# Performance work log

Measured on AMD Instinct MI355X. Metric: run time of the kernel, lower is better.

The kernel has to match this reference:

```python
import jax, jax.numpy as jnp
import numpy as np

B, S, D, H, WIN = 2, 2048, 1024, 16, 128
DH = D // H


def setup_inputs() -> dict:
    key = jax.random.key(0)
    ks = jax.random.split(key, 6)
    sc = D ** -0.5
    return {
        "x": jax.random.normal(ks[0], (B, S, D), jnp.float32),
        "in_proj_w": jax.random.normal(ks[1], (3 * D, D), jnp.float32) * sc,
        "in_proj_b": jnp.zeros((3 * D,), jnp.float32),
        "out_proj_w": jax.random.normal(ks[2], (D, D), jnp.float32) * sc,
        "out_proj_b": jnp.zeros((D,), jnp.float32),
        "ln1_g": jnp.ones((D,), jnp.float32),
        "ln1_b": jnp.zeros((D,), jnp.float32),
        "spec_wr": jax.random.normal(ks[3], (S // 2 + 1, D), jnp.float32) * 0.02 + 1.0,
        "spec_wi": jax.random.normal(ks[4], (S // 2 + 1, D), jnp.float32) * 0.02,
        "ln2_g": jnp.ones((D,), jnp.float32),
        "ln2_b": jnp.zeros((D,), jnp.float32),
    }


def _layernorm(x, g, b, eps=1e-5):
    mu = jnp.mean(x, axis=-1, keepdims=True)
    var = jnp.mean(jnp.square(x - mu), axis=-1, keepdims=True)
    return (x - mu) * jax.lax.rsqrt(var + eps) * g + b


def reference(x, in_proj_w, in_proj_b, out_proj_w, out_proj_b,
              ln1_g, ln1_b, spec_wr, spec_wi, ln2_g, ln2_b):
    b, s, d = x.shape
    # --- sliding-window MHA (torch nn.MultiheadAttention math) ---
    qkv = x @ in_proj_w.T + in_proj_b            # [B,S,3D]
    q, k, v = jnp.split(qkv, 3, axis=-1)
    q = q.reshape(b, s, H, DH)
    k = k.reshape(b, s, H, DH)
    v = v.reshape(b, s, H, DH)
    scores = jnp.einsum('bqhd,bkhd->bhqk', q, k) * (DH ** -0.5)
    idx = jnp.arange(s)
    band_mask = jnp.abs(idx[:, None] - idx[None, :]) > WIN  # True = masked
    scores = jnp.where(band_mask[None, None], -jnp.inf, scores)
    probs = jax.nn.softmax(scores, axis=-1)
    attn = jnp.einsum('bhqk,bkhd->bqhd', probs, v).reshape(b, s, d)
    attn_out = attn @ out_proj_w.T + out_proj_b
    x_attn = _layernorm(x + attn_out, ln1_g, ln1_b)
    # --- spectral block: rfft along seq, learned complex filter, irfft ---
    Xf = jnp.fft.rfft(x, axis=1)                  # [B, S//2+1, D] complex
    Wc = spec_wr + 1j * spec_wi
    x_wave = jnp.fft.irfft(Xf * Wc[None], n=s, axis=1).astype(x.dtype)
    # --- mix ---
    return _layernorm(x_attn + x_wave, ln2_g, ln2_b)
```

## Files before the change

kernel.cpp:

```cpp
#include <hip/hip_runtime.h>
#include <hip/hip_bf16.h>
#include <math.h>

#define BB    2
#define SS    2048
#define DD    1024
#define HH    16
#define DHH   64
#define WINW  128
#define MROWS (BB * SS)

typedef __attribute__((ext_vector_type(8))) short short8;
typedef __attribute__((ext_vector_type(4))) short short4v;
typedef __attribute__((ext_vector_type(4))) float floatx4;

__global__ __launch_bounds__(256) void transpose_x_cast(
    const float* __restrict__ src, float* __restrict__ dstT,
    __hip_bfloat16* __restrict__ dst_bf) {
  __shared__ float tile[64][65];
  const size_t base = (size_t)blockIdx.z * SS * DD;
  const int c0 = blockIdx.x * 64;
  const int r0 = blockIdx.y * 64;
  const int tx = threadIdx.x & 63;
  const int ty = threadIdx.x >> 6;
#pragma unroll
  for (int i = 0; i < 16; ++i) {
    const int r = ty * 16 + i;
    const float v = src[base + (size_t)(r0 + r) * DD + c0 + tx];
    tile[r][tx] = v;
    dst_bf[base + (size_t)(r0 + r) * DD + c0 + tx] = __float2bfloat16(v);
  }
  __syncthreads();
#pragma unroll
  for (int i = 0; i < 16; ++i) {
    const int c = ty * 16 + i;
    dstT[base + (size_t)(c0 + c) * SS + r0 + tx] = tile[tx][c];
  }
}

__global__ __launch_bounds__(256) void cast_w(
    const float* __restrict__ w_in, const float* __restrict__ w_out,
    __hip_bfloat16* __restrict__ o_in, __hip_bfloat16* __restrict__ o_out) {
  const int i = (blockIdx.x * 256 + threadIdx.x) * 4;
  const float* src; __hip_bfloat16* dst; int j;
  if (i < 3 * DD * DD) { src = w_in; dst = o_in; j = i; }
  else { src = w_out; dst = o_out; j = i - 3 * DD * DD; }
  const float4 v = *(const float4*)(src + j);
  dst[j + 0] = __float2bfloat16(v.x);
  dst[j + 1] = __float2bfloat16(v.y);
  dst[j + 2] = __float2bfloat16(v.z);
  dst[j + 3] = __float2bfloat16(v.w);
}

__global__ __launch_bounds__(256) void transpose_wrwi(
    const float* __restrict__ wr, const float* __restrict__ wi,
    float* __restrict__ wrT, float* __restrict__ wiT) {
  __shared__ float tile[64][65];
  const float* src = blockIdx.z ? wi : wr;
  float* dst = blockIdx.z ? wiT : wrT;
  const int R = 1025, C = DD;
  const int c0 = blockIdx.x * 64;
  const int r0 = blockIdx.y * 64;
  const int tx = threadIdx.x & 63;
  const int ty = threadIdx.x >> 6;
#pragma unroll
  for (int i = 0; i < 16; ++i) {
    const int r = ty * 16 + i;
    if (r0 + r < R) tile[r][tx] = src[(size_t)(r0 + r) * C + c0 + tx];
  }
  __syncthreads();
#pragma unroll
  for (int i = 0; i < 16; ++i) {
    const int c = ty * 16 + i;
    if (r0 + tx < R) dst[(size_t)(c0 + c) * R + r0 + tx] = tile[tx][c];
  }
}

__global__ __launch_bounds__(256) void transpose_f32(
    const float* __restrict__ src, float* __restrict__ dst, int R, int C) {
  __shared__ float tile[64][65];
  const size_t base = (size_t)blockIdx.z * R * C;
  const int c0 = blockIdx.x * 64;
  const int r0 = blockIdx.y * 64;
  const int tx = threadIdx.x & 63;
  const int ty = threadIdx.x >> 6;
#pragma unroll
  for (int i = 0; i < 16; ++i) {
    const int r = ty * 16 + i;
    tile[r][tx] = src[base + (size_t)(r0 + r) * C + c0 + tx];
  }
  __syncthreads();
#pragma unroll
  for (int i = 0; i < 16; ++i) {
    const int c = ty * 16 + i;
    dst[base + (size_t)(c0 + c) * R + r0 + tx] = tile[tx][c];
  }
}

__device__ inline void load16_lds(const __hip_bfloat16* g, __hip_bfloat16* l) {
  __builtin_amdgcn_global_load_lds(
      (const __attribute__((address_space(1))) uint32_t*)g,
      (__attribute__((address_space(3))) uint32_t*)l, 16, 0, 0);
}

#define GEMM_BODY(STORE)                                                       \
  __shared__ __attribute__((aligned(16))) __hip_bfloat16 As[128 * 32];         \
  __shared__ __attribute__((aligned(16))) __hip_bfloat16 Bs[128 * 32];         \
  const int tid  = threadIdx.x;                                                \
  const int lane = tid & 63;                                                   \
  const int wave = tid >> 6;                                                   \
  const int wrow = (wave >> 1) * 64;                                           \
  const int wcol = (wave & 1) * 64;                                            \
  int id_ = blockIdx.y * gridDim.x + blockIdx.x;                               \
  const int per_ = (gridDim.x * gridDim.y) >> 3;                               \
  id_ = (id_ & 7) * per_ + (id_ >> 3);                                         \
  const int row0 = (id_ & 31) * 128;                                           \
  const int col0 = (id_ >> 5) * 128;                                           \
  const int srow = tid >> 2;                                                   \
  const int skk  = (tid & 3) * 8;                                              \
  const int quad = lane >> 4;                                                  \
  const int l16  = lane & 15;                                                  \
  floatx4 acc[4][4] = {};                                                      \
  for (int k0 = 0; k0 < K; k0 += 32) {                                         \
    __syncthreads();                                                           \
    load16_lds(A + (size_t)(row0 + srow) * K + k0 + skk,      &As[tid * 8]);   \
    load16_lds(A + (size_t)(row0 + 64 + srow) * K + k0 + skk, &As[2048 + tid * 8]); \
    load16_lds(B + (size_t)(col0 + srow) * K + k0 + skk,      &Bs[tid * 8]);   \
    load16_lds(B + (size_t)(col0 + 64 + srow) * K + k0 + skk, &Bs[2048 + tid * 8]); \
    __syncthreads();                                                           \
    short8 af[4], bf[4];                                                       \
    _Pragma("unroll")                                                          \
    for (int i = 0; i < 4; ++i)                                                \
      af[i] = *(const short8*)&As[(wrow + i * 16 + l16) * 32 + quad * 8];      \
    _Pragma("unroll")                                                          \
    for (int j = 0; j < 4; ++j)                                                \
      bf[j] = *(const short8*)&Bs[(wcol + j * 16 + l16) * 32 + quad * 8];      \
    _Pragma("unroll")                                                          \
    for (int i = 0; i < 4; ++i)                                                \
      _Pragma("unroll")                                                        \
      for (int j = 0; j < 4; ++j)                                              \
        acc[i][j] = __builtin_amdgcn_mfma_f32_16x16x32_bf16(af[i], bf[j], acc[i][j], 0, 0, 0); \
  }                                                                            \
  _Pragma("unroll")                                                            \
  for (int i = 0; i < 4; ++i) {                                                \
    _Pragma("unroll")                                                          \
    for (int j = 0; j < 4; ++j) {                                              \
      const int col = col0 + wcol + j * 16 + l16;                              \
      const float bs = bias[col];                                              \
      _Pragma("unroll")                                                        \
      for (int r = 0; r < 4; ++r) {                                            \
        const int row = row0 + wrow + i * 16 + quad * 4 + r;                   \
        STORE;                                                                 \
      }                                                                        \
    }                                                                          \
  }

__global__ __launch_bounds__(256) void gemm_bf16_nt(
    const __hip_bfloat16* __restrict__ A, const __hip_bfloat16* __restrict__ B,
    const float* __restrict__ bias, float* __restrict__ C,
    int M, int N, int K) {
  GEMM_BODY(C[(size_t)row * N + col] = acc[i][j][r] + bs)
}

__global__ __launch_bounds__(256) void gemm_bf16_nt_bf16out(
    const __hip_bfloat16* __restrict__ A, const __hip_bfloat16* __restrict__ B,
    const float* __restrict__ bias, __hip_bfloat16* __restrict__ C,
    int M, int N, int K) {
  GEMM_BODY(C[(size_t)row * N + col] = __float2bfloat16(acc[i][j][r] + bs))
}

__global__ __launch_bounds__(256, 2) void attn_mfma(
    const __hip_bfloat16* __restrict__ qkv, __hip_bfloat16* __restrict__ attn) {
  __shared__ __attribute__((aligned(16))) __hip_bfloat16 QsA[64 * 32];
  __shared__ __attribute__((aligned(16))) __hip_bfloat16 QsB[64 * 32];
  __shared__ __attribute__((aligned(16))) __hip_bfloat16 KsA[160 * 32];
  __shared__ __attribute__((aligned(16))) __hip_bfloat16 KsB[160 * 32];
  __shared__ __attribute__((aligned(16))) __hip_bfloat16 Vt[64 * 168];
  __shared__ __attribute__((aligned(16))) __hip_bfloat16 Ps[64 * 168];

  const int tid  = threadIdx.x;
  const int lane = tid & 63;
  const int w    = tid >> 6;
  const int quad = lane >> 4;
  const int l16  = lane & 15;
  const int q0   = blockIdx.x * 64;
  const int h    = blockIdx.y;
  const int b    = blockIdx.z;
  const int kbase = q0 - WINW;

  const int r_ = tid >> 2;
  const int c8 = (tid & 3) * 8;

  {
    const __hip_bfloat16* src = qkv + ((size_t)(b * SS + q0 + r_)) * (3 * DD) + h * DHH;
    load16_lds(src + c8,      &QsA[r_ * 32 + c8]);
    load16_lds(src + 32 + c8, &QsB[r_ * 32 + c8]);
  }

  short8 qf0, qf1;
  float m_run[4] = {-1e30f, -1e30f, -1e30f, -1e30f};
  float l_run[4] = {0.f, 0.f, 0.f, 0.f};
  floatx4 ob[4] = {};

  for (int c = 0; c < 2; ++c) {
    const int ck0 = kbase + c * 160;
    __syncthreads();
#pragma unroll
    for (int it = 0; it < 3; ++it) {
      const int r = it * 64 + r_;
      if (r < 160) {
        int key = ck0 + r; key = key < 0 ? 0 : (key > SS - 1 ? SS - 1 : key);
        const __hip_bfloat16* src = qkv + ((size_t)(b * SS + key)) * (3 * DD) + DD + h * DHH;
        load16_lds(src + c8,      &KsA[r * 32 + c8]);
        load16_lds(src + 32 + c8, &KsB[r * 32 + c8]);
      }
    }
    {
      const int k4 = (tid >> 3) * 4;
      const int d8 = (tid & 7) * 8;
#pragma unroll
      for (int it = 0; it < 2; ++it) {
        const int rr = it * 128 + k4;
        if (rr < 160) {
          short8 v[4];
#pragma unroll
          for (int u = 0; u < 4; ++u) {
            int key = ck0 + rr + u; key = key < 0 ? 0 : (key > SS - 1 ? SS - 1 : key);
            v[u] = *(const short8*)(qkv + ((size_t)(b * SS + key)) * (3 * DD) + 2 * DD + h * DHH + d8);
          }
#pragma unroll
          for (int j = 0; j < 8; ++j) {
            short4v pk; pk[0] = v[0][j]; pk[1] = v[1][j]; pk[2] = v[2][j]; pk[3] = v[3][j];
            *(short4v*)&Vt[(d8 + j) * 168 + rr] = pk;
          }
        }
      }
    }
    __syncthreads();

    if (c == 0) {
      qf0 = *(const short8*)&QsA[(w * 16 + l16) * 32 + quad * 8];
      qf1 = *(const short8*)&QsB[(w * 16 + l16) * 32 + quad * 8];
    }

    floatx4 sc[10];
#pragma unroll
    for (int kt = 0; kt < 10; ++kt) {
      const short8 bk0 = *(const short8*)&KsA[(kt * 16 + l16) * 32 + quad * 8];
      const short8 bk1 = *(const short8*)&KsB[(kt * 16 + l16) * 32 + quad * 8];
      floatx4 a = {};
      a = __builtin_amdgcn_mfma_f32_16x16x32_bf16(qf0, bk0, a, 0, 0, 0);
      a = __builtin_amdgcn_mfma_f32_16x16x32_bf16(qf1, bk1, a, 0, 0, 0);
      sc[kt] = a;
    }

    float cm[4] = {-1e30f, -1e30f, -1e30f, -1e30f};
#pragma unroll
    for (int kt = 0; kt < 10; ++kt) {
      const int key = ck0 + kt * 16 + l16;
#pragma unroll
      for (int r = 0; r < 4; ++r) {
        const int qq = q0 + w * 16 + quad * 4 + r;
        const int dqk = qq - key;
        const bool ok = (key >= 0) & (key < SS) & (dqk <= WINW) & (dqk >= -WINW);
        const float s = ok ? sc[kt][r] * 0.125f : -1e30f;
        sc[kt][r] = s;
        cm[r] = fmaxf(cm[r], s);
      }
    }
#pragma unroll
    for (int off = 1; off < 16; off <<= 1)
#pragma unroll
      for (int r = 0; r < 4; ++r) cm[r] = fmaxf(cm[r], __shfl_xor(cm[r], off, 64));

    float alpha[4], csum[4] = {0.f, 0.f, 0.f, 0.f};
#pragma unroll
    for (int r = 0; r < 4; ++r) {
      const float mn = fmaxf(m_run[r], cm[r]);
      alpha[r] = __expf(m_run[r] - mn);
      m_run[r] = mn;
    }

    __hip_bfloat16* Pw = &Ps[w * 16 * 168];
#pragma unroll
    for (int kt = 0; kt < 10; ++kt) {
#pragma unroll
      for (int r = 0; r < 4; ++r) {
        const float p = __expf(sc[kt][r] - m_run[r]);
        csum[r] += p;
        Pw[(quad * 4 + r) * 168 + kt * 16 + l16] = __float2bfloat16(p);
      }
    }
#pragma unroll
    for (int off = 1; off < 16; off <<= 1)
#pragma unroll
      for (int r = 0; r < 4; ++r) csum[r] += __shfl_xor(csum[r], off, 64);
#pragma unroll
    for (int r = 0; r < 4; ++r) l_run[r] = l_run[r] * alpha[r] + csum[r];
#pragma unroll
    for (int t = 0; t < 4; ++t)
#pragma unroll
      for (int r = 0; r < 4; ++r) ob[t][r] *= alpha[r];

#pragma unroll
    for (int kt = 0; kt < 5; ++kt) {
      const short8 pf = *(const short8*)&Pw[l16 * 168 + kt * 32 + quad * 8];
#pragma unroll
      for (int t = 0; t < 4; ++t) {
        const short8 vf = *(const short8*)&Vt[(t * 16 + l16) * 168 + kt * 32 + quad * 8];
        ob[t] = __builtin_amdgcn_mfma_f32_16x16x32_bf16(pf, vf, ob[t], 0, 0, 0);
      }
    }
  }

  float inv[4];
#pragma unroll
  for (int r = 0; r < 4; ++r) inv[r] = 1.f / l_run[r];
  const int qq0 = q0 + w * 16 + quad * 4;
#pragma unroll
  for (int t = 0; t < 4; ++t)
#pragma unroll
    for (int r = 0; r < 4; ++r)
      attn[((size_t)(b * SS + qq0 + r)) * DD + h * DHH + t * 16 + l16] =
          __float2bfloat16(ob[t][r] * inv[r]);
}

__global__ __launch_bounds__(256) void add_ln(
    const float* __restrict__ a, const float* __restrict__ b,
    const float* __restrict__ g, const float* __restrict__ be,
    float* __restrict__ out) {
  const int row = blockIdx.x;
  const int tid = threadIdx.x;
  const int lane = tid & 63;
  const int wave = tid >> 6;

  const float4 av = *(const float4*)(a + (size_t)row * DD + tid * 4);
  const float4 bv = *(const float4*)(b + (size_t)row * DD + tid * 4);
  float v[4] = {av.x + bv.x, av.y + bv.y, av.z + bv.z, av.w + bv.w};

  float s = v[0] + v[1] + v[2] + v[3];
  float s2 = v[0] * v[0] + v[1] * v[1] + v[2] * v[2] + v[3] * v[3];
#pragma unroll
  for (int off = 32; off; off >>= 1) {
    s += __shfl_xor(s, off, 64);
    s2 += __shfl_xor(s2, off, 64);
  }
  __shared__ float red[8];
  if (lane == 0) { red[wave] = s; red[4 + wave] = s2; }
  __syncthreads();
  s = red[0] + red[1] + red[2] + red[3];
  s2 = red[4] + red[5] + red[6] + red[7];

  const float mu = s * (1.f / DD);
  const float var = s2 * (1.f / DD) - mu * mu;
  const float r = rsqrtf(var + 1e-5f);

  const float4 gv = *(const float4*)(g + tid * 4);
  const float4 bev = *(const float4*)(be + tid * 4);
  float4 o;
  o.x = (v[0] - mu) * r * gv.x + bev.x;
  o.y = (v[1] - mu) * r * gv.y + bev.y;
  o.z = (v[2] - mu) * r * gv.z + bev.z;
  o.w = (v[3] - mu) * r * gv.w + bev.w;
  *(float4*)(out + (size_t)row * DD + tid * 4) = o;
}

#define PADI(a) ((a) + ((a) >> 5))

__global__ __launch_bounds__(256) void spec_fft_pair(
    float* __restrict__ xT, const float* __restrict__ wrT,
    const float* __restrict__ wiT) {
  __shared__ float re[SS + SS / 32], im[SS + SS / 32];
  const int tid = threadIdx.x;
  const int d0 = blockIdx.x * 2, d1 = d0 + 1;
  const int b = blockIdx.y;
  float* col0 = xT + ((size_t)b * DD + d0) * SS;
  float* col1 = xT + ((size_t)b * DD + d1) * SS;

  for (int s4 = tid * 4; s4 < SS; s4 += 1024) {
    const float4 a = *(const float4*)(col0 + s4);
    const float4 c = *(const float4*)(col1 + s4);
    const int p = PADI(s4);
    re[p] = a.x; re[p + 1] = a.y; re[p + 2] = a.z; re[p + 3] = a.w;
    im[p] = c.x; im[p + 1] = c.y; im[p + 2] = c.z; im[p + 3] = c.w;
  }

  for (int stage = 11; stage >= 1; --stage) {
    __syncthreads();
    const int half = 1 << (stage - 1);
    const float ang0 = -6.283185307179586f / (float)(1 << stage);
#pragma unroll 4
    for (int t = tid; t < SS / 2; t += 256) {
      const int gI = t >> (stage - 1);
      const int p = t & (half - 1);
      const int i = (gI << stage) + p;
      const int j = i + half;
      float sn, cs;
      __sincosf(ang0 * (float)p, &sn, &cs);
      const int ii = PADI(i), jj = PADI(j);
      const float ar = re[ii], ai = im[ii], br = re[jj], bi = im[jj];
      re[ii] = ar + br; im[ii] = ai + bi;
      const float dr = ar - br, di = ai - bi;
      re[jj] = dr * cs - di * sn;
      im[jj] = dr * sn + di * cs;
    }
  }
  __syncthreads();

  const float* w0r = wrT + (size_t)d0 * 1025;
  const float* w0i = wiT + (size_t)d0 * 1025;
  const float* w1r = wrT + (size_t)d1 * 1025;
  const float* w1i = wiT + (size_t)d1 * 1025;
  const float sc = 1.0f / (float)SS;
  for (int k = tid; k < 1024; k += 256) {
    if (k == 0) {
      re[0] *= w0r[0] * sc;
      im[0] *= w1r[0] * sc;
      re[1] *= w0r[1024] * sc;
      im[1] *= w1r[1024] * sc;
    } else {
      const int p1 = PADI(__brev((unsigned)k) >> 21);
      const int p2 = PADI(__brev((unsigned)(SS - k)) >> 21);
      const float ra = re[p1], ia = im[p1];
      const float rb = re[p2], ib = im[p2];
      const float z0r = 0.5f * (ra + rb), z0i = 0.5f * (ia - ib);
      const float z1r = 0.5f * (ia + ib), z1i = -0.5f * (ra - rb);
      const float a0 = w0r[k] * sc, b0 = w0i[k] * sc;
      const float a1 = w1r[k] * sc, b1 = w1i[k] * sc;
      const float y0r = z0r * a0 - z0i * b0, y0i = z0r * b0 + z0i * a0;
      const float y1r = z1r * a1 - z1i * b1, y1i = z1r * b1 + z1i * a1;
      re[p1] = y0r - y1i; im[p1] = y0i + y1r;
      re[p2] = y0r + y1i; im[p2] = y1r - y0i;
    }
  }

  for (int stage = 1; stage <= 11; ++stage) {
    __syncthreads();
    const int half = 1 << (stage - 1);
    const float ang0 = 6.283185307179586f / (float)(1 << stage);
#pragma unroll 4
    for (int t = tid; t < SS / 2; t += 256) {
      const int gI = t >> (stage - 1);
      const int p = t & (half - 1);
      const int i = (gI << stage) + p;
      const int j = i + half;
      float sn, cs;
      __sincosf(ang0 * (float)p, &sn, &cs);
      const int ii = PADI(i), jj = PADI(j);
      const float br = re[jj], bi = im[jj];
      const float tr = br * cs - bi * sn;
      const float ti = br * sn + bi * cs;
      const float ar = re[ii], ai = im[ii];
      re[ii] = ar + tr; im[ii] = ai + ti;
      re[jj] = ar - tr; im[jj] = ai - ti;
    }
  }
  __syncthreads();

  for (int s4 = tid * 4; s4 < SS; s4 += 1024) {
    const int p = PADI(s4);
    float4 a, c;
    a.x = re[p]; a.y = re[p + 1]; a.z = re[p + 2]; a.w = re[p + 3];
    c.x = im[p]; c.y = im[p + 1]; c.z = im[p + 2]; c.w = im[p + 3];
    *(float4*)(col0 + s4) = a;
    *(float4*)(col1 + s4) = c;
  }
}

extern "C" void kernel_launch(void* const* d_in, const int* in_sizes, int n_in,
                              void* d_out, int out_size, void* d_ws, size_t ws_size,
                              hipStream_t stream) {
  const float* x     = (const float*)d_in[0];
  const float* in_w  = (const float*)d_in[1];
  const float* in_b  = (const float*)d_in[2];
  const float* out_w = (const float*)d_in[3];
  const float* out_b = (const float*)d_in[4];
  const float* ln1_g = (const float*)d_in[5];
  const float* ln1_b = (const float*)d_in[6];
  const float* wr    = (const float*)d_in[7];
  const float* wi    = (const float*)d_in[8];
  const float* ln2_g = (const float*)d_in[9];
  const float* ln2_b = (const float*)d_in[10];
  float* out = (float*)d_out;

  char* ws = (char*)d_ws;
  float* xT                = (float*)(ws);
  __hip_bfloat16* x_bf     = (__hip_bfloat16*)(ws + 16777216);
  __hip_bfloat16* w_in_bf  = (__hip_bfloat16*)(ws + 25165824);
  __hip_bfloat16* w_out_bf = (__hip_bfloat16*)(ws + 31457280);
  float* x_attn            = (float*)(ws + 16777216);
  __hip_bfloat16* qkv_bf   = (__hip_bfloat16*)(ws + 33554432);
  __hip_bfloat16* attn_bf  = (__hip_bfloat16*)(ws + 58720256);
  float* attn_out          = (float*)(ws + 33554432);
  float* wrT               = (float*)(ws + 33554432);
  float* wiT               = (float*)(ws + 37752832);
  float* x_wave            = (float*)(ws + 46137344);

  transpose_x_cast<<<dim3(16, 32, 2), 256, 0, stream>>>(x, xT, x_bf);

  cast_w<<<4096, 256, 0, stream>>>(in_w, out_w, w_in_bf, w_out_bf);

  gemm_bf16_nt_bf16out<<<dim3(3072 / 128, MROWS / 128), 256, 0, stream>>>(
      x_bf, w_in_bf, in_b, qkv_bf, MROWS, 3 * DD, DD);

  attn_mfma<<<dim3(SS / 64, HH, BB), 256, 0, stream>>>(qkv_bf, attn_bf);

  gemm_bf16_nt<<<dim3(DD / 128, MROWS / 128), 256, 0, stream>>>(
      attn_bf, w_out_bf, out_b, attn_out, MROWS, DD, DD);

  add_ln<<<MROWS, 256, 0, stream>>>(x, attn_out, ln1_g, ln1_b, x_attn);

  transpose_wrwi<<<dim3(16, 17, 2), 256, 0, stream>>>(wr, wi, wrT, wiT);

  spec_fft_pair<<<dim3(DD / 2, BB), 256, 0, stream>>>(xT, wrT, wiT);

  transpose_f32<<<dim3(32, 16, 2), 256, 0, stream>>>(xT, x_wave, DD, SS);

  add_ln<<<MROWS, 256, 0, stream>>>(x_attn, x_wave, ln2_g, ln2_b, out);
}
```

Baseline: 257.7 us.

## Co-schedule spectral FFT with QKV GEMM, fuse transpose-back and both layernorms

Merges the spectral FFT blocks into the same launch as the QKV GEMM (a heterogeneous grid of 1792 blocks) and the x_wave transpose-back into the output-projection GEMM launch. The two add+layernorm kernels become one that computes both norms per row. Intermediates (spectral weights, attn_out, x_wave) are stored in bf16 to cut memory traffic. The goal is fewer launches and better GPU fill by overlapping independent work, at the cost of bf16 rounding on the spectral filter and residual paths and more complex dispatch.

```diff
diff --git a/kernel.cpp b/kernel.cpp
--- a/kernel.cpp
+++ b/kernel.cpp
@@ -13,6 +13,12 @@
 typedef __attribute__((ext_vector_type(8))) short short8;
 typedef __attribute__((ext_vector_type(4))) short short4v;
 typedef __attribute__((ext_vector_type(4))) float floatx4;
+
+__device__ __forceinline__ float bf2f(short s) {
+  union { unsigned u; float f; } t;
+  t.u = ((unsigned)(unsigned short)s) << 16;
+  return t.f;
+}
 
 __global__ __launch_bounds__(256) void transpose_x_cast(
     const float* __restrict__ src, float* __restrict__ dstT,
@@ -52,12 +58,12 @@
   dst[j + 3] = __float2bfloat16(v.w);
 }
 
-__global__ __launch_bounds__(256) void transpose_wrwi(
+__global__ __launch_bounds__(256) void transpose_wrwi_bf(
     const float* __restrict__ wr, const float* __restrict__ wi,
-    float* __restrict__ wrT, float* __restrict__ wiT) {
+    __hip_bfloat16* __restrict__ wrT, __hip_bfloat16* __restrict__ wiT) {
   __shared__ float tile[64][65];
   const float* src = blockIdx.z ? wi : wr;
-  float* dst = blockIdx.z ? wiT : wrT;
+  __hip_bfloat16* dst = blockIdx.z ? wiT : wrT;
   const int R = 1025, C = DD;
   const int c0 = blockIdx.x * 64;
   const int r0 = blockIdx.y * 64;
@@ -72,28 +78,7 @@
 #pragma unroll
   for (int i = 0; i < 16; ++i) {
     const int c = ty * 16 + i;
-    if (r0 + tx < R) dst[(size_t)(c0 + c) * R + r0 + tx] = tile[tx][c];
-  }
-}
-
-__global__ __launch_bounds__(256) void transpose_f32(
-    const float* __restrict__ src, float* __restrict__ dst, int R, int C) {
-  __shared__ float tile[64][65];
-  const size_t base = (size_t)blockIdx.z * R * C;
-  const int c0 = blockIdx.x * 64;
-  const int r0 = blockIdx.y * 64;
-  const int tx = threadIdx.x & 63;
-  const int ty = threadIdx.x >> 6;
-#pragma unroll
-  for (int i = 0; i < 16; ++i) {
-    const int r = ty * 16 + i;
-    tile[r][tx] = src[base + (size_t)(r0 + r) * C + c0 + tx];
-  }
-  __syncthreads();
-#pragma unroll
-  for (int i = 0; i < 16; ++i) {
-    const int c = ty * 16 + i;
-    dst[base + (size_t)(c0 + c) * R + r0 + tx] = tile[tx][c];
+    if (r0 + tx < R) dst[(size_t)(c0 + c) * R + r0 + tx] = __float2bfloat16(tile[tx][c]);
   }
 }
 
@@ -103,277 +88,72 @@
       (__attribute__((address_space(3))) uint32_t*)l, 16, 0, 0);
 }
 
-#define GEMM_BODY(STORE)                                                       \
-  __shared__ __attribute__((aligned(16))) __hip_bfloat16 As[128 * 32];         \
-  __shared__ __attribute__((aligned(16))) __hip_bfloat16 Bs[128 * 32];         \
-  const int tid  = threadIdx.x;                                                \
-  const int lane = tid & 63;                                                   \
-  const int wave = tid >> 6;                                                   \
-  const int wrow = (wave >> 1) * 64;                                           \
-  const int wcol = (wave & 1) * 64;                                            \
-  int id_ = blockIdx.y * gridDim.x + blockIdx.x;                               \
-  const int per_ = (gridDim.x * gridDim.y) >> 3;                               \
-  id_ = (id_ & 7) * per_ + (id_ >> 3);                                         \
-  const int row0 = (id_ & 31) * 128;                                           \
-  const int col0 = (id_ >> 5) * 128;                                           \
-  const int srow = tid >> 2;                                                   \
-  const int skk  = (tid & 3) * 8;                                              \
-  const int quad = lane >> 4;                                                  \
-  const int l16  = lane & 15;                                                  \
-  floatx4 acc[4][4] = {};                                                      \
-  for (int k0 = 0; k0 < K; k0 += 32) {                                         \
-    __syncthreads();                                                           \
-    load16_lds(A + (size_t)(row0 + srow) * K + k0 + skk,      &As[tid * 8]);   \
-    load16_lds(A + (size_t)(row0 + 64 + srow) * K + k0 + skk, &As[2048 + tid * 8]); \
-    load16_lds(B + (size_t)(col0 + srow) * K + k0 + skk,      &Bs[tid * 8]);   \
-    load16_lds(B + (size_t)(col0 + 64 + srow) * K + k0 + skk, &Bs[2048 + tid * 8]); \
-    __syncthreads();                                                           \
-    short8 af[4], bf[4];                                                       \
-    _Pragma("unroll")                                                          \
-    for (int i = 0; i < 4; ++i)                                                \
-      af[i] = *(const short8*)&As[(wrow + i * 16 + l16) * 32 + quad * 8];      \
-    _Pragma("unroll")                                                          \
-    for (int j = 0; j < 4; ++j)                                                \
-      bf[j] = *(const short8*)&Bs[(wcol + j * 16 + l16) * 32 + quad * 8];      \
-    _Pragma("unroll")                                                          \
-    for (int i = 0; i < 4; ++i)                                                \
-      _Pragma("unroll")                                                        \
-      for (int j = 0; j < 4; ++j)                                              \
-        acc[i][j] = __builtin_amdgcn_mfma_f32_16x16x32_bf16(af[i], bf[j], acc[i][j], 0, 0, 0); \
-  }                                                                            \
-  _Pragma("unroll")                                                            \
-  for (int i = 0; i < 4; ++i) {                                                \
-    _Pragma("unroll")                                                          \
-    for (int j = 0; j < 4; ++j) {                                              \
-      const int col = col0 + wcol + j * 16 + l16;                              \
-      const float bs = bias[col];                                              \
-      _Pragma("unroll")                                                        \
-      for (int r = 0; r < 4; ++r) {                                            \
-        const int row = row0 + wrow + i * 16 + quad * 4 + r;                   \
-        STORE;                                                                 \
-      }                                                                        \
-    }                                                                          \
-  }
-
-__global__ __launch_bounds__(256) void gemm_bf16_nt(
+template <bool BF16OUT>
+__device__ __forceinline__ void gemm_tile128(
     const __hip_bfloat16* __restrict__ A, const __hip_bfloat16* __restrict__ B,
-    const float* __restrict__ bias, float* __restrict__ C,
-    int M, int N, int K) {
-  GEMM_BODY(C[(size_t)row * N + col] = acc[i][j][r] + bs)
-}
-
-__global__ __launch_bounds__(256) void gemm_bf16_nt_bf16out(
-    const __hip_bfloat16* __restrict__ A, const __hip_bfloat16* __restrict__ B,
-    const float* __restrict__ bias, __hip_bfloat16* __restrict__ C,
-    int M, int N, int K) {
-  GEMM_BODY(C[(size_t)row * N + col] = __float2bfloat16(acc[i][j][r] + bs))
-}
-
-__global__ __launch_bounds__(256, 2) void attn_mfma(
-    const __hip_bfloat16* __restrict__ qkv, __hip_bfloat16* __restrict__ attn) {
-  __shared__ __attribute__((aligned(16))) __hip_bfloat16 QsA[64 * 32];
-  __shared__ __attribute__((aligned(16))) __hip_bfloat16 QsB[64 * 32];
-  __shared__ __attribute__((aligned(16))) __hip_bfloat16 KsA[160 * 32];
-  __shared__ __attribute__((aligned(16))) __hip_bfloat16 KsB[160 * 32];
-  __shared__ __attribute__((aligned(16))) __hip_bfloat16 Vt[64 * 168];
-  __shared__ __attribute__((aligned(16))) __hip_bfloat16 Ps[64 * 168];
-
+    const float* __restrict__ bias, void* __restrict__ Cp,
+    int N, int K, int row0, int col0,
+    __hip_bfloat16* As, __hip_bfloat16* Bs) {
   const int tid  = threadIdx.x;
   const int lane = tid & 63;
-  const int w    = tid >> 6;
+  const int wave = tid >> 6;
+  const int wrow = (wave >> 1) * 64;
+  const int wcol = (wave & 1) * 64;
+  const int srow = tid >> 2;
+  const int skk  = (tid & 3) * 8;
   const int quad = lane >> 4;
   const int l16  = lane & 15;
-  const int q0   = blockIdx.x * 64;
-  const int h    = blockIdx.y;
-  const int b    = blockIdx.z;
-  const int kbase = q0 - WINW;
-
-  const int r_ = tid >> 2;
-  const int c8 = (tid & 3) * 8;
-
-  {
-    const __hip_bfloat16* src = qkv + ((size_t)(b * SS + q0 + r_)) * (3 * DD) + h * DHH;
-    load16_lds(src + c8,      &QsA[r_ * 32 + c8]);
-    load16_lds(src + 32 + c8, &QsB[r_ * 32 + c8]);
-  }
-
-  short8 qf0, qf1;
-  float m_run[4] = {-1e30f, -1e30f, -1e30f, -1e30f};
-  float l_run[4] = {0.f, 0.f, 0.f, 0.f};
-  floatx4 ob[4] = {};
-
-  for (int c = 0; c < 2; ++c) {
-    const int ck0 = kbase + c * 160;
-    __syncthreads();
-#pragma unroll
-    for (int it = 0; it < 3; ++it) {
-      const int r = it * 64 + r_;
-      if (r < 160) {
-        int key = ck0 + r; key = key < 0 ? 0 : (key > SS - 1 ? SS - 1 : key);
-        const __hip_bfloat16* src = qkv + ((size_t)(b * SS + key)) * (3 * DD) + DD + h * DHH;
-        load16_lds(src + c8,      &KsA[r * 32 + c8]);
-        load16_lds(src + 32 + c8, &KsB[r * 32 + c8]);
+  floatx4 acc[4][4] = {};
+  for (int k0 = 0; k0 < K; k0 += 32) {
+    __syncthreads();
+    load16_lds(A + (size_t)(row0 + srow) * K + k0 + skk,      &As[tid * 8]);
+    load16_lds(A + (size_t)(row0 + 64 + srow) * K + k0 + skk, &As[2048 + tid * 8]);
+    load16_lds(B + (size_t)(col0 + srow) * K + k0 + skk,      &Bs[tid * 8]);
+    load16_lds(B + (size_t)(col0 + 64 + srow) * K + k0 + skk, &Bs[2048 + tid * 8]);
+    __syncthreads();
+    short8 af[4], bf[4];
+#pragma unroll
+    for (int i = 0; i < 4; ++i)
+      af[i] = *(const short8*)&As[(wrow + i * 16 + l16) * 32 + quad * 8];
+#pragma unroll
+    for (int j = 0; j < 4; ++j)
+      bf[j] = *(const short8*)&Bs[(wcol + j * 16 + l16) * 32 + quad * 8];
+#pragma unroll
+    for (int i = 0; i < 4; ++i)
+#pragma unroll
+      for (int j = 0; j < 4; ++j)
+        acc[i][j] = __builtin_amdgcn_mfma_f32_16x16x32_bf16(af[i], bf[j], acc[i][j], 0, 0, 0);
+  }
+#pragma unroll
+  for (int i = 0; i < 4; ++i) {
+#pragma unroll
+    for (int j = 0; j < 4; ++j) {
+      const int col = col0 + wcol + j * 16 + l16;
+      const float bs = bias[col];
+#pragma unroll
+      for (int r = 0; r < 4; ++r) {
+        const int row = row0 + wrow + i * 16 + quad * 4 + r;
+        if (BF16OUT)
+          ((__hip_bfloat16*)Cp)[(size_t)row * N + col] = __float2bfloat16(acc[i][j][r] + bs);
+        else
+          ((float*)Cp)[(size_t)row * N + col] = acc[i][j][r] + bs;
       }
     }
-    {
-      const int k4 = (tid >> 3) * 4;
-      const int d8 = (tid & 7) * 8;
-#pragma unroll
-      for (int it = 0; it < 2; ++it) {
-        const int rr = it * 128 + k4;
-        if (rr < 160) {
-          short8 v[4];
-#pragma unroll
-          for (int u = 0; u < 4; ++u) {
-            int key = ck0 + rr + u; key = key < 0 ? 0 : (key > SS - 1 ? SS - 1 : key);
-            v[u] = *(const short8*)(qkv + ((size_t)(b * SS + key)) * (3 * DD) + 2 * DD + h * DHH + d8);
-          }
-#pragma unroll
-          for (int j = 0; j < 8; ++j) {
-            short4v pk; pk[0] = v[0][j]; pk[1] = v[1][j]; pk[2] = v[2][j]; pk[3] = v[3][j];
-            *(short4v*)&Vt[(d8 + j) * 168 + rr] = pk;
-          }
-        }
-      }
-    }
-    __syncthreads();
-
-    if (c == 0) {
-      qf0 = *(const short8*)&QsA[(w * 16 + l16) * 32 + quad * 8];
-      qf1 = *(const short8*)&QsB[(w * 16 + l16) * 32 + quad * 8];
-    }
-
-    floatx4 sc[10];
-#pragma unroll
-    for (int kt = 0; kt < 10; ++kt) {
-      const short8 bk0 = *(const short8*)&KsA[(kt * 16 + l16) * 32 + quad * 8];
-      const short8 bk1 = *(const short8*)&KsB[(kt * 16 + l16) * 32 + quad * 8];
-      floatx4 a = {};
-      a = __builtin_amdgcn_mfma_f32_16x16x32_bf16(qf0, bk0, a, 0, 0, 0);
-      a = __builtin_amdgcn_mfma_f32_16x16x32_bf16(qf1, bk1, a, 0, 0, 0);
-      sc[kt] = a;
-    }
-
-    float cm[4] = {-1e30f, -1e30f, -1e30f, -1e30f};
-#pragma unroll
-    for (int kt = 0; kt < 10; ++kt) {
-      const int key = ck0 + kt * 16 + l16;
-#pragma unroll
-      for (int r = 0; r < 4; ++r) {
-        const int qq = q0 + w * 16 + quad * 4 + r;
-        const int dqk = qq - key;
-        const bool ok = (key >= 0) & (key < SS) & (dqk <= WINW) & (dqk >= -WINW);
-        const float s = ok ? sc[kt][r] * 0.125f : -1e30f;
-        sc[kt][r] = s;
-        cm[r] = fmaxf(cm[r], s);
-      }
-    }
-#pragma unroll
-    for (int off = 1; off < 16; off <<= 1)
-#pragma unroll
-      for (int r = 0; r < 4; ++r) cm[r] = fmaxf(cm[r], __shfl_xor(cm[r], off, 64));
-
-    float alpha[4], csum[4] = {0.f, 0.f, 0.f, 0.f};
-#pragma unroll
-    for (int r = 0; r < 4; ++r) {
-      const float mn = fmaxf(m_run[r], cm[r]);
-      alpha[r] = __expf(m_run[r] - mn);
-      m_run[r] = mn;
-    }
-
-    __hip_bfloat16* Pw = &Ps[w * 16 * 168];
-#pragma unroll
-    for (int kt = 0; kt < 10; ++kt) {
-#pragma unroll
-      for (int r = 0; r < 4; ++r) {
-        const float p = __expf(sc[kt][r] - m_run[r]);
-        csum[r] += p;
-        Pw[(quad * 4 + r) * 168 + kt * 16 + l16] = __float2bfloat16(p);
-      }
-    }
-#pragma unroll
-    for (int off = 1; off < 16; off <<= 1)
-#pragma unroll
-      for (int r = 0; r < 4; ++r) csum[r] += __shfl_xor(csum[r], off, 64);
-#pragma unroll
-    for (int r = 0; r < 4; ++r) l_run[r] = l_run[r] * alpha[r] + csum[r];
-#pragma unroll
-    for (int t = 0; t < 4; ++t)
-#pragma unroll
-      for (int r = 0; r < 4; ++r) ob[t][r] *= alpha[r];
-
-#pragma unroll
-    for (int kt = 0; kt < 5; ++kt) {
-      const short8 pf = *(const short8*)&Pw[l16 * 168 + kt * 32 + quad * 8];
-#pragma unroll
-      for (int t = 0; t < 4; ++t) {
-        const short8 vf = *(const short8*)&Vt[(t * 16 + l16) * 168 + kt * 32 + quad * 8];
-        ob[t] = __builtin_amdgcn_mfma_f32_16x16x32_bf16(pf, vf, ob[t], 0, 0, 0);
-      }
-    }
-  }
-
-  float inv[4];
-#pragma unroll
-  for (int r = 0; r < 4; ++r) inv[r] = 1.f / l_run[r];
-  const int qq0 = q0 + w * 16 + quad * 4;
-#pragma unroll
-  for (int t = 0; t < 4; ++t)
-#pragma unroll
-    for (int r = 0; r < 4; ++r)
-      attn[((size_t)(b * SS + qq0 + r)) * DD + h * DHH + t * 16 + l16] =
-          __float2bfloat16(ob[t][r] * inv[r]);
-}
-
-__global__ __launch_bounds__(256) void add_ln(
-    const float* __restrict__ a, const float* __restrict__ b,
-    const float* __restrict__ g, const float* __restrict__ be,
-    float* __restrict__ out) {
-  const int row = blockIdx.x;
+  }
+}
+
+#define PADI(a) ((a) + ((a) >> 5))
+
+__device__ __forceinline__ void spec_body(
+    int sid, float* __restrict__ xT,
+    const __hip_bfloat16* __restrict__ wrT, const __hip_bfloat16* __restrict__ wiT,
+    float* sm) {
+  float* re = sm;
+  float* im = sm + 2112;
   const int tid = threadIdx.x;
-  const int lane = tid & 63;
-  const int wave = tid >> 6;
-
-  const float4 av = *(const float4*)(a + (size_t)row * DD + tid * 4);
-  const float4 bv = *(const float4*)(b + (size_t)row * DD + tid * 4);
-  float v[4] = {av.x + bv.x, av.y + bv.y, av.z + bv.z, av.w + bv.w};
-
-  float s = v[0] + v[1] + v[2] + v[3];
-  float s2 = v[0] * v[0] + v[1] * v[1] + v[2] * v[2] + v[3] * v[3];
-#pragma unroll
-  for (int off = 32; off; off >>= 1) {
-    s += __shfl_xor(s, off, 64);
-    s2 += __shfl_xor(s2, off, 64);
-  }
-  __shared__ float red[8];
-  if (lane == 0) { red[wave] = s; red[4 + wave] = s2; }
-  __syncthreads();
-  s = red[0] + red[1] + red[2] + red[3];
-  s2 = red[4] + red[5] + red[6] + red[7];
-
-  const float mu = s * (1.f / DD);
-  const float var = s2 * (1.f / DD) - mu * mu;
-  const float r = rsqrtf(var + 1e-5f);
-
-  const float4 gv = *(const float4*)(g + tid * 4);
-  const float4 bev = *(const float4*)(be + tid * 4);
-  float4 o;
-  o.x = (v[0] - mu) * r * gv.x + bev.x;
-  o.y = (v[1] - mu) * r * gv.y + bev.y;
-  o.z = (v[2] - mu) * r * gv.z + bev.z;
-  o.w = (v[3] - mu) * r * gv.w + bev.w;
-  *(float4*)(out + (size_t)row * DD + tid * 4) = o;
-}
-
-#define PADI(a) ((a) + ((a) >> 5))
-
-__global__ __launch_bounds__(256) void spec_fft_pair(
-    float* __restrict__ xT, const float* __restrict__ wrT,
-    const float* __restrict__ wiT) {
-  __shared__ float re[SS + SS / 32], im[SS + SS / 32];
-  const int tid = threadIdx.x;
-  const int d0 = blockIdx.x * 2, d1 = d0 + 1;
-  const int b = blockIdx.y;
+  const int dpair = sid & 511;
+  const int b = sid >> 9;
+  const int d0 = dpair * 2, d1 = d0 + 1;
   float* col0 = xT + ((size_t)b * DD + d0) * SS;
   float* col1 = xT + ((size_t)b * DD + d1) * SS;
 
@@ -407,17 +187,17 @@
   }
   __syncthreads();
 
-  const float* w0r = wrT + (size_t)d0 * 1025;
-  const float* w0i = wiT + (size_t)d0 * 1025;
-  const float* w1r = wrT + (size_t)d1 * 1025;
-  const float* w1i = wiT + (size_t)d1 * 1025;
+  const __hip_bfloat16* w0r = wrT + (size_t)d0 * 1025;
+  const __hip_bfloat16* w0i = wiT + (size_t)d0 * 1025;
+  const __hip_bfloat16* w1r = wrT + (size_t)d1 * 1025;
+  const __hip_bfloat16* w1i = wiT + (size_t)d1 * 1025;
   const float sc = 1.0f / (float)SS;
   for (int k = tid; k < 1024; k += 256) {
     if (k == 0) {
-      re[0] *= w0r[0] * sc;
-      im[0] *= w1r[0] * sc;
-      re[1] *= w0r[1024] * sc;
-      im[1] *= w1r[1024] * sc;
+      re[0] *= __bfloat162float(w0r[0]) * sc;
+      im[0] *= __bfloat162float(w1r[0]) * sc;
+      re[1] *= __bfloat162float(w0r[1024]) * sc;
+      im[1] *= __bfloat162float(w1r[1024]) * sc;
     } else {
       const int p1 = PADI(__brev((unsigned)k) >> 21);
       const int p2 = PADI(__brev((unsigned)(SS - k)) >> 21);
@@ -425,8 +205,8 @@
       const float rb = re[p2], ib = im[p2];
       const float z0r = 0.5f * (ra + rb), z0i = 0.5f * (ia - ib);
       const float z1r = 0.5f * (ia + ib), z1i = -0.5f * (ra - rb);
-      const float a0 = w0r[k] * sc, b0 = w0i[k] * sc;
-      const float a1 = w1r[k] * sc, b1 = w1i[k] * sc;
+      const float a0 = __bfloat162float(w0r[k]) * sc, b0 = __bfloat162float(w0i[k]) * sc;
+      const float a1 = __bfloat162float(w1r[k]) * sc, b1 = __bfloat162float(w1i[k]) * sc;
       const float y0r = z0r * a0 - z0i * b0, y0i = z0r * b0 + z0i * a0;
       const float y1r = z1r * a1 - z1i * b1, y1i = z1r * b1 + z1i * a1;
       re[p1] = y0r - y1i; im[p1] = y0i + y1r;
@@ -467,6 +247,282 @@
   }
 }
 
+__global__ __launch_bounds__(256) void gemm1_spec(
+    const __hip_bfloat16* __restrict__ x_bf, const __hip_bfloat16* __restrict__ w_in_bf,
+    const float* __restrict__ in_b, __hip_bfloat16* __restrict__ qkv_bf,
+    float* __restrict__ xT, const __hip_bfloat16* __restrict__ wrT,
+    const __hip_bfloat16* __restrict__ wiT) {
+  extern __shared__ __align__(16) char smem[];
+  if (blockIdx.x < 768) {
+    const int id = blockIdx.x;
+    const int col0 = (id % 24) * 128;
+    const int row0 = (id / 24) * 128;
+    gemm_tile128<true>(x_bf, w_in_bf, in_b, qkv_bf, 3 * DD, DD, row0, col0,
+                       (__hip_bfloat16*)smem, (__hip_bfloat16*)smem + 4096);
+  } else {
+    spec_body(blockIdx.x - 768, xT, wrT, wiT, (float*)smem);
+  }
+}
+
+__global__ __launch_bounds__(256) void gemm2_tback(
+    const __hip_bfloat16* __restrict__ attn_bf, const __hip_bfloat16* __restrict__ w_out_bf,
+    const float* __restrict__ out_b, __hip_bfloat16* __restrict__ attn_out_bf,
+    const float* __restrict__ xT, __hip_bfloat16* __restrict__ x_wave_bf) {
+  extern __shared__ __align__(16) char smem[];
+  if (blockIdx.x < 256) {
+    const int id = blockIdx.x;
+    const int col0 = (id % 8) * 128;
+    const int row0 = (id / 8) * 128;
+    gemm_tile128<true>(attn_bf, w_out_bf, out_b, attn_out_bf, DD, DD, row0, col0,
+                       (__hip_bfloat16*)smem, (__hip_bfloat16*)smem + 4096);
+  } else {
+    float (*tile)[65] = (float(*)[65])smem;
+    const int id = blockIdx.x - 256;
+    const int bz = id >> 9;
+    const int rem = id & 511;
+    const int s0 = (rem >> 4) * 64;
+    const int d0 = (rem & 15) * 64;
+    const int tx = threadIdx.x & 63;
+    const int ty = threadIdx.x >> 6;
+    const float* src = xT + (size_t)bz * DD * SS;
+    __hip_bfloat16* dst = x_wave_bf + (size_t)bz * SS * DD;
+#pragma unroll
+    for (int i = 0; i < 16; ++i) {
+      const int r = ty * 16 + i;
+      tile[r][tx] = src[(size_t)(d0 + r) * SS + s0 + tx];
+    }
+    __syncthreads();
+#pragma unroll
+    for (int i = 0; i < 16; ++i) {
+      const int c = ty * 16 + i;
+      dst[(size_t)(s0 + c) * DD + d0 + tx] = __float2bfloat16(tile[tx][c]);
+    }
+  }
+}
+
+__global__ __launch_bounds__(256, 2) void attn_mfma(
+    const __hip_bfloat16* __restrict__ qkv, __hip_bfloat16* __restrict__ attn) {
+  __shared__ __attribute__((aligned(16))) __hip_bfloat16 QsA[64 * 32];
+  __shared__ __attribute__((aligned(16))) __hip_bfloat16 QsB[64 * 32];
+  __shared__ __attribute__((aligned(16))) __hip_bfloat16 KsA[160 * 32];
+  __shared__ __attribute__((aligned(16))) __hip_bfloat16 KsB[160 * 32];
+  __shared__ __attribute__((aligned(16))) __hip_bfloat16 Vt[64 * 168];
+  __shared__ __attribute__((aligned(16))) __hip_bfloat16 Ps[64 * 168];
+
+  const int tid  = threadIdx.x;
+  const int lane = tid & 63;
+  const int w    = tid >> 6;
+  const int quad = lane >> 4;
+  const int l16  = lane & 15;
+  const int q0   = blockIdx.x * 64;
+  const int h    = blockIdx.y;
+  const int b    = blockIdx.z;
+  const int kbase = q0 - WINW;
+
+  const int r_ = tid >> 2;
+  const int c8 = (tid & 3) * 8;
+
+  {
+    const __hip_bfloat16* src = qkv + ((size_t)(b * SS + q0 + r_)) * (3 * DD) + h * DHH;
+    load16_lds(src + c8,      &QsA[r_ * 32 + c8]);
+    load16_lds(src + 32 + c8, &QsB[r_ * 32 + c8]);
+  }
+
+  short8 qf0, qf1;
+  float m_run[4] = {-1e30f, -1e30f, -1e30f, -1e30f};
+  float l_run[4] = {0.f, 0.f, 0.f, 0.f};
+  floatx4 ob[4] = {};
+
+  for (int c = 0; c < 2; ++c) {
+    const int ck0 = kbase + c * 160;
+    __syncthreads();
+#pragma unroll
+    for (int it = 0; it < 3; ++it) {
+      const int r = it * 64 + r_;
+      if (r < 160) {
+        int key = ck0 + r; key = key < 0 ? 0 : (key > SS - 1 ? SS - 1 : key);
+        const __hip_bfloat16* src = qkv + ((size_t)(b * SS + key)) * (3 * DD) + DD + h * DHH;
+        load16_lds(src + c8,      &KsA[r * 32 + c8]);
+        load16_lds(src + 32 + c8, &KsB[r * 32 + c8]);
+      }
+    }
+    {
+      const int k4 = (tid >> 3) * 4;
+      const int d8 = (tid & 7) * 8;
+#pragma unroll
+      for (int it = 0; it < 2; ++it) {
+        const int rr = it * 128 + k4;
+        if (rr < 160) {
+          short8 v[4];
+#pragma unroll
+          for (int u = 0; u < 4; ++u) {
+            int key = ck0 + rr + u; key = key < 0 ? 0 : (key > SS - 1 ? SS - 1 : key);
+            v[u] = *(const short8*)(qkv + ((size_t)(b * SS + key)) * (3 * DD) + 2 * DD + h * DHH + d8);
+          }
+#pragma unroll
+          for (int j = 0; j < 8; ++j) {
+            short4v pk; pk[0] = v[0][j]; pk[1] = v[1][j]; pk[2] = v[2][j]; pk[3] = v[3][j];
+            *(short4v*)&Vt[(d8 + j) * 168 + rr] = pk;
+          }
+        }
+      }
+    }
+    __syncthreads();
+
+    if (c == 0) {
+      qf0 = *(const short8*)&QsA[(w * 16 + l16) * 32 + quad * 8];
+      qf1 = *(const short8*)&QsB[(w * 16 + l16) * 32 + quad * 8];
+    }
+
+    floatx4 sc[10];
+#pragma unroll
+    for (int kt = 0; kt < 10; ++kt) {
+      const short8 bk0 = *(const short8*)&KsA[(kt * 16 + l16) * 32 + quad * 8];
+      const short8 bk1 = *(const short8*)&KsB[(kt * 16 + l16) * 32 + quad * 8];
+      floatx4 a = {};
+      a = __builtin_amdgcn_mfma_f32_16x16x32_bf16(qf0, bk0, a, 0, 0, 0);
+      a = __builtin_amdgcn_mfma_f32_16x16x32_bf16(qf1, bk1, a, 0, 0, 0);
+      sc[kt] = a;
+    }
+
+    float cm[4] = {-1e30f, -1e30f, -1e30f, -1e30f};
+#pragma unroll
+    for (int kt = 0; kt < 10; ++kt) {
+      const int key = ck0 + kt * 16 + l16;
+#pragma unroll
+      for (int r = 0; r < 4; ++r) {
+        const int qq = q0 + w * 16 + quad * 4 + r;
+        const int dqk = qq - key;
+        const bool ok = (key >= 0) & (key < SS) & (dqk <= WINW) & (dqk >= -WINW);
+        const float s = ok ? sc[kt][r] * 0.125f : -1e30f;
+        sc[kt][r] = s;
+        cm[r] = fmaxf(cm[r], s);
+      }
+    }
+#pragma unroll
+    for (int off = 1; off < 16; off <<= 1)
+#pragma unroll
+      for (int r = 0; r < 4; ++r) cm[r] = fmaxf(cm[r], __shfl_xor(cm[r], off, 64));
+
+    float alpha[4], csum[4] = {0.f, 0.f, 0.f, 0.f};
+#pragma unroll
+    for (int r = 0; r < 4; ++r) {
+      const float mn = fmaxf(m_run[r], cm[r]);
+      alpha[r] = __expf(m_run[r] - mn);
+      m_run[r] = mn;
+    }
+
+    __hip_bfloat16* Pw = &Ps[w * 16 * 168];
+#pragma unroll
+    for (int kt = 0; kt < 10; ++kt) {
+#pragma unroll
+      for (int r = 0; r < 4; ++r) {
+        const float p = __expf(sc[kt][r] - m_run[r]);
+        csum[r] += p;
+        Pw[(quad * 4 + r) * 168 + kt * 16 + l16] = __float2bfloat16(p);
+      }
+    }
+#pragma unroll
+    for (int off = 1; off < 16; off <<= 1)
+#pragma unroll
+      for (int r = 0; r < 4; ++r) csum[r] += __shfl_xor(csum[r], off, 64);
+#pragma unroll
+    for (int r = 0; r < 4; ++r) l_run[r] = l_run[r] * alpha[r] + csum[r];
+#pragma unroll
+    for (int t = 0; t < 4; ++t)
+#pragma unroll
+      for (int r = 0; r < 4; ++r) ob[t][r] *= alpha[r];
+
+#pragma unroll
+    for (int kt = 0; kt < 5; ++kt) {
+      const short8 pf = *(const short8*)&Pw[l16 * 168 + kt * 32 + quad * 8];
+#pragma unroll
+      for (int t = 0; t < 4; ++t) {
+        const short8 vf = *(const short8*)&Vt[(t * 16 + l16) * 168 + kt * 32 + quad * 8];
+        ob[t] = __builtin_amdgcn_mfma_f32_16x16x32_bf16(pf, vf, ob[t], 0, 0, 0);
+      }
+    }
+  }
+
+  float inv[4];
+#pragma unroll
+  for (int r = 0; r < 4; ++r) inv[r] = 1.f / l_run[r];
+  const int qq0 = q0 + w * 16 + quad * 4;
+#pragma unroll
+  for (int t = 0; t < 4; ++t)
+#pragma unroll
+    for (int r = 0; r < 4; ++r)
+      attn[((size_t)(b * SS + qq0 + r)) * DD + h * DHH + t * 16 + l16] =
+          __float2bfloat16(ob[t][r] * inv[r]);
+}
+
+__global__ __launch_bounds__(256) void ln_fused(
+    const float* __restrict__ x, const __hip_bfloat16* __restrict__ attn_out,
+    const float* __restrict__ g1, const float* __restrict__ b1,
+    const __hip_bfloat16* __restrict__ xwave,
+    const float* __restrict__ g2, const float* __restrict__ b2,
+    float* __restrict__ out) {
+  const int row = blockIdx.x;
+  const int tid = threadIdx.x;
+  const int lane = tid & 63;
+  const int wave = tid >> 6;
+  __shared__ float red[8];
+
+  const float4 xv = *(const float4*)(x + (size_t)row * DD + tid * 4);
+  const short4v av = *(const short4v*)(attn_out + (size_t)row * DD + tid * 4);
+  float v[4] = {xv.x + bf2f(av[0]), xv.y + bf2f(av[1]),
+                xv.z + bf2f(av[2]), xv.w + bf2f(av[3])};
+
+  float s = v[0] + v[1] + v[2] + v[3];
+  float s2 = v[0] * v[0] + v[1] * v[1] + v[2] * v[2] + v[3] * v[3];
+#pragma unroll
+  for (int off = 32; off; off >>= 1) {
+    s += __shfl_xor(s, off, 64);
+    s2 += __shfl_xor(s2, off, 64);
+  }
+  if (lane == 0) { red[wave] = s; red[4 + wave] = s2; }
+  __syncthreads();
+  s = red[0] + red[1] + red[2] + red[3];
+  s2 = red[4] + red[5] + red[6] + red[7];
+  float mu = s * (1.f / DD);
+  float var = s2 * (1.f / DD) - mu * mu;
+  float r = rsqrtf(var + 1e-5f);
+
+  const float4 g1v = *(const float4*)(g1 + tid * 4);
+  const float4 b1v = *(const float4*)(b1 + tid * 4);
+  const short4v wv = *(const short4v*)(xwave + (size_t)row * DD + tid * 4);
+  float a[4];
+  a[0] = (v[0] - mu) * r * g1v.x + b1v.x + bf2f(wv[0]);
+  a[1] = (v[1] - mu) * r * g1v.y + b1v.y + bf2f(wv[1]);
+  a[2] = (v[2] - mu) * r * g1v.z + b1v.z + bf2f(wv[2]);
+  a[3] = (v[3] - mu) * r * g1v.w + b1v.w + bf2f(wv[3]);
+
+  s = a[0] + a[1] + a[2] + a[3];
+  s2 = a[0] * a[0] + a[1] * a[1] + a[2] * a[2] + a[3] * a[3];
+#pragma unroll
+  for (int off = 32; off; off >>= 1) {
+    s += __shfl_xor(s, off, 64);
+    s2 += __shfl_xor(s2, off, 64);
+  }
+  __syncthreads();
+  if (lane == 0) { red[wave] = s; red[4 + wave] = s2; }
+  __syncthreads();
+  s = red[0] + red[1] + red[2] + red[3];
+  s2 = red[4] + red[5] + red[6] + red[7];
+  mu = s * (1.f / DD);
+  var = s2 * (1.f / DD) - mu * mu;
+  r = rsqrtf(var + 1e-5f);
+
+  const float4 g2v = *(const float4*)(g2 + tid * 4);
+  const float4 b2v = *(const float4*)(b2 + tid * 4);
+  float4 o;
+  o.x = (a[0] - mu) * r * g2v.x + b2v.x;
+  o.y = (a[1] - mu) * r * g2v.y + b2v.y;
+  o.z = (a[2] - mu) * r * g2v.z + b2v.z;
+  o.w = (a[3] - mu) * r * g2v.w + b2v.w;
+  *(float4*)(out + (size_t)row * DD + tid * 4) = o;
+}
+
 extern "C" void kernel_launch(void* const* d_in, const int* in_sizes, int n_in,
                               void* d_out, int out_size, void* d_ws, size_t ws_size,
                               hipStream_t stream) {
@@ -486,35 +542,29 @@
   char* ws = (char*)d_ws;
   float* xT                = (float*)(ws);
   __hip_bfloat16* x_bf     = (__hip_bfloat16*)(ws + 16777216);
+  __hip_bfloat16* attn_bf  = (__hip_bfloat16*)(ws + 16777216);
   __hip_bfloat16* w_in_bf  = (__hip_bfloat16*)(ws + 25165824);
   __hip_bfloat16* w_out_bf = (__hip_bfloat16*)(ws + 31457280);
-  float* x_attn            = (float*)(ws + 16777216);
   __hip_bfloat16* qkv_bf   = (__hip_bfloat16*)(ws + 33554432);
-  __hip_bfloat16* attn_bf  = (__hip_bfloat16*)(ws + 58720256);
-  float* attn_out          = (float*)(ws + 33554432);
-  float* wrT               = (float*)(ws + 33554432);
-  float* wiT               = (float*)(ws + 37752832);
-  float* x_wave            = (float*)(ws + 46137344);
+  __hip_bfloat16* attn_out_bf = (__hip_bfloat16*)(ws + 33554432);
+  __hip_bfloat16* x_wave_bf   = (__hip_bfloat16*)(ws + 44040192);
+  __hip_bfloat16* wrT      = (__hip_bfloat16*)(ws + 58720256);
+  __hip_bfloat16* wiT      = (__hip_bfloat16*)(ws + 60819456);
 
   transpose_x_cast<<<dim3(16, 32, 2), 256, 0, stream>>>(x, xT, x_bf);
 
   cast_w<<<4096, 256, 0, stream>>>(in_w, out_w, w_in_bf, w_out_bf);
 
-  gemm_bf16_nt_bf16out<<<dim3(3072 / 128, MROWS / 128), 256, 0, stream>>>(
-      x_bf, w_in_bf, in_b, qkv_bf, MROWS, 3 * DD, DD);
+  transpose_wrwi_bf<<<dim3(16, 17, 2), 256, 0, stream>>>(wr, wi, wrT, wiT);
+
+  gemm1_spec<<<1792, 256, 16896, stream>>>(x_bf, w_in_bf, in_b, qkv_bf,
+                                           xT, wrT, wiT);
 
   attn_mfma<<<dim3(SS / 64, HH, BB), 256, 0, stream>>>(qkv_bf, attn_bf);
 
-  gemm_bf16_nt<<<dim3(DD / 128, MROWS / 128), 256, 0, stream>>>(
-      attn_bf, w_out_bf, out_b, attn_out, MROWS, DD, DD);
-
-  add_ln<<<MROWS, 256, 0, stream>>>(x, attn_out, ln1_g, ln1_b, x_attn);
-
-  transpose_wrwi<<<dim3(16, 17, 2), 256, 0, stream>>>(wr, wi, wrT, wiT);
-
-  spec_fft_pair<<<dim3(DD / 2, BB), 256, 0, stream>>>(xT, wrT, wiT);
-
-  transpose_f32<<<dim3(32, 16, 2), 256, 0, stream>>>(xT, x_wave, DD, SS);
-
-  add_ln<<<MROWS, 256, 0, stream>>>(x_attn, x_wave, ln2_g, ln2_b, out);
-}
+  gemm2_tback<<<1280, 256, 16640, stream>>>(attn_bf, w_out_bf, out_b,
+                                            attn_out_bf, xT, x_wave_bf);
+
+  ln_fused<<<MROWS, 256, 0, stream>>>(x, attn_out_bf, ln1_g, ln1_b,
+                                      x_wave_bf, ln2_g, ln2_b, out);
+}
```

After: 232.6 us. 1.11x faster.
